# Kernel tuning notes

Measured on AMD Instinct MI355X. Metric: run time of the kernel, lower is better.

Reference implementation:

```python
import jax, jax.numpy as jnp
import numpy as np

L = 2          # layer_num
B = 8192       # nframes * nloc
NNEI = 128
EMB = 128
HID = 128
SHIFT = 20.0   # attnw_shift default
SCALING = (HID * 1.0) ** (-0.5)
LN_EPS = 1e-5


def _l2norm(x):
    # torch F.normalize: x / max(||x||, 1e-12)
    n = jnp.sqrt(jnp.sum(x * x, axis=-1, keepdims=True))
    return x / jnp.maximum(n, 1e-12)


def _layernorm(x, g, b):
    mu = jnp.mean(x, axis=-1, keepdims=True)
    var = jnp.mean((x - mu) ** 2, axis=-1, keepdims=True)
    return (x - mu) * jax.lax.rsqrt(var + LN_EPS) * g + b


def setup_inputs() -> dict:
    key = jax.random.key(0)
    ks = jax.random.split(key, 10)
    input_G = jax.random.normal(ks[0], (B, NNEI, EMB), dtype=jnp.float32)
    nei_mask = jax.random.randint(ks[1], (B, NNEI), 0, 2) > 0
    input_r = jax.random.normal(ks[2], (B, NNEI, 3), dtype=jnp.float32)
    input_r = _l2norm(input_r)  # normalized radial vectors
    sw = jax.random.uniform(ks[3], (B, NNEI), dtype=jnp.float32)
    s = 0.02
    W_in = jax.random.normal(ks[4], (L, EMB, 3 * HID), dtype=jnp.float32) * s
    b_in = jnp.zeros((L, 3 * HID), dtype=jnp.float32)
    W_out = jax.random.normal(ks[5], (L, HID, EMB), dtype=jnp.float32) * s
    b_out = jnp.zeros((L, EMB), dtype=jnp.float32)
    ln_g = jnp.ones((L, EMB), dtype=jnp.float32)
    ln_b = jnp.zeros((L, EMB), dtype=jnp.float32)
    return {"input_G": input_G, "nei_mask": nei_mask, "input_r": input_r,
            "sw": sw, "W_in": W_in, "b_in": b_in, "W_out": W_out,
            "b_out": b_out, "ln_g": ln_g, "ln_b": ln_b}


def reference(input_G, nei_mask, input_r, sw, W_in, b_in, W_out, b_out, ln_g, ln_b):
    # smooth=True, dotr=True path of NeighborGatedAttention
    sw_ij = sw[:, :, None] * sw[:, None, :]                     # [B, nnei, nnei]
    ang = jnp.einsum('bnc,bmc->bnm', input_r, input_r)          # angular weight
    x = input_G
    for l in range(L):
        residual = x
        qkv = jnp.einsum('bne,eh->bnh', x, W_in[l]) + b_in[l]
        q, k, v = jnp.split(qkv, 3, axis=-1)
        q = _l2norm(q) * SCALING
        k = _l2norm(k)
        v = _l2norm(v)
        attn = jnp.einsum('bnh,bmh->bnm', q, k)
        attn = (attn + SHIFT) * sw_ij - SHIFT                   # switch smoothing
        attn = jax.nn.softmax(attn, axis=-1)
        attn = jnp.where(nei_mask[:, :, None], attn, 0.0)       # zero masked rows
        attn = attn * sw_ij * ang                               # smooth + dotr
        o = jnp.einsum('bnm,bmh->bnh', attn, v)
        out = jnp.einsum('bnh,he->bne', o, W_out[l]) + b_out[l]
        x = _layernorm(residual + out, ln_g[l], ln_b[l])
    return x
```

## Files before the change

### kernel.cpp

```cpp
#include <hip/hip_runtime.h>
#include <hip/hip_bf16.h>
#include <math.h>


typedef __attribute__((ext_vector_type(8))) short bf16x8;
typedef __attribute__((ext_vector_type(4))) float f32x4;
typedef unsigned short ushort_t;

constexpr float F_SHIFT   = 20.0f;
constexpr float F_SCALING = 0.08838834764831845f;
constexpr float F_LNEPS   = 1e-5f;

constexpr int ROWP = 136;
constexpr int BUF_US = 128 * ROWP;
constexpr size_t WTI_ELEMS = 2 * 384 * 128;
constexpr size_t WTO_ELEMS = 2 * 128 * 128;
constexpr int TAB_F = 1920;
constexpr int LDS_BYTES = 4 * BUF_US * 2 + 2 * TAB_F * 4;

#define MFMA(a, b, c) __builtin_amdgcn_mfma_f32_16x16x32_bf16(a, b, c, 0, 0, 0)

__device__ __forceinline__ ushort_t f2bf(float f) {
  __hip_bfloat16 h = __float2bfloat16(f);
  return *reinterpret_cast<ushort_t*>(&h);
}
__device__ __forceinline__ ushort4 pack4(float a, float b, float c, float d) {
  return make_ushort4(f2bf(a), f2bf(b), f2bf(c), f2bf(d));
}

template <bool WS>
__device__ __forceinline__ bf16x8 wt_frag(const ushort_t* __restrict__ wt,
                                          const float* __restrict__ W,
                                          int r, int c, int ldW) {
  if constexpr (WS) {
    return *(const bf16x8*)(wt + r * 128 + c);
  } else {
    bf16x8 f;
#pragma unroll
    for (int j = 0; j < 8; ++j) f[j] = (short)f2bf(W[(size_t)(c + j) * ldW + r]);
    return f;
  }
}

__global__ void prep_weights(const float* __restrict__ Win, const float* __restrict__ Wout,
                             ushort_t* __restrict__ wtI, ushort_t* __restrict__ wtO) {
  const int i = blockIdx.x * 256 + threadIdx.x;
  if (i < (int)WTI_ELEMS) {
    const int l = i / (384 * 128), r = i % (384 * 128), h = r >> 7, e = r & 127;
    wtI[i] = f2bf(Win[l * (128 * 384) + e * 384 + h]);
  }
  if (i < (int)WTO_ELEMS) {
    const int l = i >> 14, r = i & 16383, e = r >> 7, h = r & 127;
    wtO[i] = f2bf(Wout[(l << 14) + h * 128 + e]);
  }
}

__device__ __forceinline__ bf16x8 load_xf(const float* xr) {
  const float4 a = *(const float4*)xr;
  const float4 c = *(const float4*)(xr + 4);
  bf16x8 f;
  f[0] = (short)f2bf(a.x); f[1] = (short)f2bf(a.y);
  f[2] = (short)f2bf(a.z); f[3] = (short)f2bf(a.w);
  f[4] = (short)f2bf(c.x); f[5] = (short)f2bf(c.y);
  f[6] = (short)f2bf(c.z); f[7] = (short)f2bf(c.w);
  return f;
}

template <bool WS>
__global__ __launch_bounds__(512, 2)
void ngatt_dual(const float* __restrict__ G, const int* __restrict__ nmask,
                const float* __restrict__ r3, const float* __restrict__ swg,
                const float* __restrict__ Win, const float* __restrict__ bin,
                const float* __restrict__ Wout, const float* __restrict__ bout,
                const float* __restrict__ lng, const float* __restrict__ lnb,
                const ushort_t* __restrict__ wtin, const ushort_t* __restrict__ wtout,
                float* __restrict__ xout) {
  extern __shared__ char smem[];
  ushort_t* bufA0 = (ushort_t*)smem;
  ushort_t* bufB0 = bufA0 + BUF_US;
  ushort_t* bufA1 = bufB0 + BUF_US;
  ushort_t* bufB1 = bufA1 + BUF_US;
  float* tab0 = (float*)(bufB1 + BUF_US);
  float* tab1 = tab0 + TAB_F;

  const int bid = blockIdx.x, t = threadIdx.x;
  const int w = t >> 6, l = t & 63, lc = l & 15, lg = l >> 4;
  const int b0 = 2 * bid, b1 = b0 + 1;
  const size_t bb0 = (size_t)b0 * (128 * 128);
  const size_t bb1 = (size_t)b1 * (128 * 128);
  const int n_mine = 16 * w + lc;

  if (t < 256) {
    const int tb = t >> 7, tt = t & 127;
    float* T = tb ? tab1 : tab0;
    const size_t gi = (size_t)(b0 + tb) * 128 + tt;
    T[1280 + tt] = swg[gi];
    T[1408 + tt] = nmask[gi] ? 1.0f : 0.0f;
    T[1536 + tt] = r3[gi * 3 + 0];
    T[1664 + tt] = r3[gi * 3 + 1];
    T[1792 + tt] = r3[gi * 3 + 2];
  }
  __syncthreads();

  for (int layer = 0; layer < 2; ++layer) {
    const float* xsrc0 = layer ? (xout + bb0) : (G + bb0);
    const float* xsrc1 = layer ? (xout + bb1) : (G + bb1);
    const ushort_t* wtI = wtin + (size_t)layer * 384 * 128;
    const ushort_t* wtO = wtout + (size_t)layer * 128 * 128;
    const float* WinL  = Win  + (size_t)layer * 128 * 384;
    const float* WoutL = Wout + (size_t)layer * 128 * 128;
    const float* binL  = bin  + layer * 384;
    const float* boutL = bout + layer * 128;
    const float* lngL  = lng  + layer * 128;
    const float* lnbL  = lnb  + layer * 128;

    bf16x8 xf0[4], xf1[4];
#pragma unroll
    for (int kk = 0; kk < 4; ++kk) {
      xf0[kk] = load_xf(xsrc0 + (size_t)n_mine * 128 + 8 * lg + 32 * kk);
      xf1[kk] = load_xf(xsrc1 + (size_t)n_mine * 128 + 8 * lg + 32 * kk);
    }

    float ssq0 = 0.f, ssq1 = 0.f, ssk0 = 0.f, ssk1 = 0.f;
#pragma unroll 2
    for (int i = 0; i < 8; ++i) {
      bf16x8 aw[4];
#pragma unroll
      for (int kk = 0; kk < 4; ++kk)
        aw[kk] = wt_frag<WS>(wtI, WinL, 16 * i + lc, 8 * lg + 32 * kk, 384);
      f32x4 a0 = {0, 0, 0, 0}, a1 = {0, 0, 0, 0};
#pragma unroll
      for (int kk = 0; kk < 4; ++kk) {
        a0 = MFMA(aw[kk], xf0[kk], a0);
        a1 = MFMA(aw[kk], xf1[kk], a1);
      }
      const float4 bi = *(const float4*)&binL[16 * i + 4 * lg];
      {
        const float v0 = a0[0] + bi.x, v1 = a0[1] + bi.y, v2 = a0[2] + bi.z, v3 = a0[3] + bi.w;
        ssq0 += v0 * v0 + v1 * v1 + v2 * v2 + v3 * v3;
        *(ushort4*)(bufA0 + n_mine * ROWP + 16 * i + 4 * lg) = pack4(v0, v1, v2, v3);
      }
      {
        const float v0 = a1[0] + bi.x, v1 = a1[1] + bi.y, v2 = a1[2] + bi.z, v3 = a1[3] + bi.w;
        ssq1 += v0 * v0 + v1 * v1 + v2 * v2 + v3 * v3;
        *(ushort4*)(bufA1 + n_mine * ROWP + 16 * i + 4 * lg) = pack4(v0, v1, v2, v3);
      }
    }
#pragma unroll 2
    for (int i = 0; i < 8; ++i) {
      bf16x8 aw[4];
#pragma unroll
      for (int kk = 0; kk < 4; ++kk)
        aw[kk] = wt_frag<WS>(wtI, WinL, 128 + 16 * i + lc, 8 * lg + 32 * kk, 384);
      f32x4 a0 = {0, 0, 0, 0}, a1 = {0, 0, 0, 0};
#pragma unroll
      for (int kk = 0; kk < 4; ++kk) {
        a0 = MFMA(aw[kk], xf0[kk], a0);
        a1 = MFMA(aw[kk], xf1[kk], a1);
      }
      const float4 bi = *(const float4*)&binL[128 + 16 * i + 4 * lg];
      {
        const float v0 = a0[0] + bi.x, v1 = a0[1] + bi.y, v2 = a0[2] + bi.z, v3 = a0[3] + bi.w;
        ssk0 += v0 * v0 + v1 * v1 + v2 * v2 + v3 * v3;
        *(ushort4*)(bufB0 + n_mine * ROWP + 16 * i + 4 * lg) = pack4(v0, v1, v2, v3);
      }
      {
        const float v0 = a1[0] + bi.x, v1 = a1[1] + bi.y, v2 = a1[2] + bi.z, v3 = a1[3] + bi.w;
        ssk1 += v0 * v0 + v1 * v1 + v2 * v2 + v3 * v3;
        *(ushort4*)(bufB1 + n_mine * ROWP + 16 * i + 4 * lg) = pack4(v0, v1, v2, v3);
      }
    }
    ssq0 += __shfl_xor(ssq0, 16); ssq0 += __shfl_xor(ssq0, 32);
    ssq1 += __shfl_xor(ssq1, 16); ssq1 += __shfl_xor(ssq1, 32);
    ssk0 += __shfl_xor(ssk0, 16); ssk0 += __shfl_xor(ssk0, 32);
    ssk1 += __shfl_xor(ssk1, 16); ssk1 += __shfl_xor(ssk1, 32);
    if (l < 16) {
      tab0[0 + n_mine] = ssq0; tab0[128 + n_mine] = ssk0;
      tab1[0 + n_mine] = ssq1; tab1[128 + n_mine] = ssk1;
    }
    __syncthreads();

    if (t < 256) {
      const int tb = t >> 7, tt = t & 127;
      float* T = tb ? tab1 : tab0;
      T[0 + tt] = 1.0f / fmaxf(sqrtf(T[0 + tt]), 1e-12f);
      T[512 + 4 * tt + 0] = (1.0f / fmaxf(sqrtf(T[128 + tt]), 1e-12f)) * F_SCALING;
      T[512 + 4 * tt + 1] = T[1280 + tt];
      T[512 + 4 * tt + 2] = 0.0f;
      T[512 + 4 * tt + 3] = T[1536 + tt];
      T[1024 + 2 * tt + 0] = T[1664 + tt];
      T[1024 + 2 * tt + 1] = T[1792 + tt];
    }
    bf16x8 qf0[4], qf1[4];
#pragma unroll
    for (int kk = 0; kk < 4; ++kk) {
      qf0[kk] = *(const bf16x8*)(bufA0 + n_mine * ROWP + 8 * lg + 32 * kk);
      qf1[kk] = *(const bf16x8*)(bufA1 + n_mine * ROWP + 8 * lg + 32 * kk);
    }
    __syncthreads();

    float ssv0 = 0.f, ssv1 = 0.f;
#pragma unroll 2
    for (int i = 0; i < 8; ++i) {
      bf16x8 aw[4];
#pragma unroll
      for (int kk = 0; kk < 4; ++kk)
        aw[kk] = wt_frag<WS>(wtI, WinL, 256 + 16 * i + lc, 8 * lg + 32 * kk, 384);
      f32x4 a0 = {0, 0, 0, 0}, a1 = {0, 0, 0, 0};
#pragma unroll
      for (int kk = 0; kk < 4; ++kk) {
        a0 = MFMA(aw[kk], xf0[kk], a0);
        a1 = MFMA(aw[kk], xf1[kk], a1);
      }
      const float4 bi = *(const float4*)&binL[256 + 16 * i + 4 * lg];
      {
        const float v0 = a0[0] + bi.x, v1 = a0[1] + bi.y, v2 = a0[2] + bi.z, v3 = a0[3] + bi.w;
        ssv0 += v0 * v0 + v1 * v1 + v2 * v2 + v3 * v3;
        *(ushort4*)(bufA0 + n_mine * ROWP + 16 * i + 4 * lg) = pack4(v0, v1, v2, v3);
      }
      {
        const float v0 = a1[0] + bi.x, v1 = a1[1] + bi.y, v2 = a1[2] + bi.z, v3 = a1[3] + bi.w;
        ssv1 += v0 * v0 + v1 * v1 + v2 * v2 + v3 * v3;
        *(ushort4*)(bufA1 + n_mine * ROWP + 16 * i + 4 * lg) = pack4(v0, v1, v2, v3);
      }
    }
    ssv0 += __shfl_xor(ssv0, 16); ssv0 += __shfl_xor(ssv0, 32);
    ssv1 += __shfl_xor(ssv1, 16); ssv1 += __shfl_xor(ssv1, 32);
    if (l < 16) { tab0[256 + n_mine] = ssv0; tab1[256 + n_mine] = ssv1; }

    ushort4 p0[8], p1[8];
    {
      const float iqn = tab0[0 + n_mine];
      const float swn = tab0[1280 + n_mine];
      const float rxn = tab0[1536 + n_mine], ryn = tab0[1664 + n_mine], rzn = tab0[1792 + n_mine];
      float sum = 0.0f;
      f32x4 sacc[8];
#pragma unroll 2
      for (int mt = 0; mt < 8; ++mt) {
        bf16x8 kf[4];
#pragma unroll
        for (int kk = 0; kk < 4; ++kk)
          kf[kk] = *(const bf16x8*)(bufB0 + (16 * mt + lc) * ROWP + 8 * lg + 32 * kk);
        __builtin_amdgcn_s_setprio(1);
        f32x4 a = {0, 0, 0, 0};
#pragma unroll
        for (int kk = 0; kk < 4; ++kk) a = MFMA(kf[kk], qf0[kk], a);
        __builtin_amdgcn_s_setprio(0);
#pragma unroll
        for (int r2 = 0; r2 < 4; ++r2) {
          const int m = 16 * mt + 4 * lg + r2;
          const float4 a4 = *(const float4*)&tab0[512 + 4 * m];
          const float2 b2 = *(const float2*)&tab0[1024 + 2 * m];
          const float sws = swn * a4.y;
          const float e = __expf((a[r2] * iqn * a4.x + F_SHIFT) * sws - F_SHIFT);
          sum += e;
          a[r2] = e * sws * (rxn * a4.w + ryn * b2.x + rzn * b2.y);
        }
        sacc[mt] = a;
      }
      sum += __shfl_xor(sum, 16); sum += __shfl_xor(sum, 32);
      const float fac = tab0[1408 + n_mine] / sum;
#pragma unroll
      for (int mt = 0; mt < 8; ++mt)
        p0[mt] = pack4(sacc[mt][0] * fac, sacc[mt][1] * fac, sacc[mt][2] * fac, sacc[mt][3] * fac);
    }
    {
      const float iqn = tab1[0 + n_mine];
      const float swn = tab1[1280 + n_mine];
      const float rxn = tab1[1536 + n_mine], ryn = tab1[1664 + n_mine], rzn = tab1[1792 + n_mine];
      float sum = 0.0f;
      f32x4 sacc[8];
#pragma unroll 2
      for (int mt = 0; mt < 8; ++mt) {
        bf16x8 kf[4];
#pragma unroll
        for (int kk = 0; kk < 4; ++kk)
          kf[kk] = *(const bf16x8*)(bufB1 + (16 * mt + lc) * ROWP + 8 * lg + 32 * kk);
        __builtin_amdgcn_s_setprio(1);
        f32x4 a = {0, 0, 0, 0};
#pragma unroll
        for (int kk = 0; kk < 4; ++kk) a = MFMA(kf[kk], qf1[kk], a);
        __builtin_amdgcn_s_setprio(0);
#pragma unroll
        for (int r2 = 0; r2 < 4; ++r2) {
          const int m = 16 * mt + 4 * lg + r2;
          const float4 a4 = *(const float4*)&tab1[512 + 4 * m];
          const float2 b2 = *(const float2*)&tab1[1024 + 2 * m];
          const float sws = swn * a4.y;
          const float e = __expf((a[r2] * iqn * a4.x + F_SHIFT) * sws - F_SHIFT);
          sum += e;
          a[r2] = e * sws * (rxn * a4.w + ryn * b2.x + rzn * b2.y);
        }
        sacc[mt] = a;
      }
      sum += __shfl_xor(sum, 16); sum += __shfl_xor(sum, 32);
      const float fac = tab1[1408 + n_mine] / sum;
#pragma unroll
      for (int mt = 0; mt < 8; ++mt)
        p1[mt] = pack4(sacc[mt][0] * fac, sacc[mt][1] * fac, sacc[mt][2] * fac, sacc[mt][3] * fac);
    }
    __syncthreads();

    if (t < 256) {
      const int tb = t >> 7, tt = t & 127;
      float* T = tb ? tab1 : tab0;
      T[384 + tt] = 1.0f / fmaxf(sqrtf(T[256 + tt]), 1e-12f);
    }
#pragma unroll
    for (int mt = 0; mt < 8; ++mt) {
      *(ushort4*)(bufB0 + n_mine * ROWP + 16 * mt + 4 * lg) = p0[mt];
      *(ushort4*)(bufB1 + n_mine * ROWP + 16 * mt + 4 * lg) = p1[mt];
    }
    bf16x8 vf0[4], vf1[4];
#pragma unroll
    for (int kk = 0; kk < 4; ++kk) {
      vf0[kk] = *(const bf16x8*)(bufA0 + n_mine * ROWP + 8 * lg + 32 * kk);
      vf1[kk] = *(const bf16x8*)(bufA1 + n_mine * ROWP + 8 * lg + 32 * kk);
    }
    __syncthreads();

    {
      const float4 iv0 = *(const float4*)&tab0[384 + 16 * w + 4 * lg];
      const float4 iv1 = *(const float4*)&tab1[384 + 16 * w + 4 * lg];
#pragma unroll 2
      for (int i = 0; i < 8; ++i) {
        bf16x8 bw[4];
#pragma unroll
        for (int kk = 0; kk < 4; ++kk)
          bw[kk] = wt_frag<WS>(wtO, WoutL, 16 * i + lc, 8 * lg + 32 * kk, 128);
        f32x4 a0 = {0, 0, 0, 0}, a1 = {0, 0, 0, 0};
#pragma unroll
        for (int kk = 0; kk < 4; ++kk) {
          a0 = MFMA(vf0[kk], bw[kk], a0);
          a1 = MFMA(vf1[kk], bw[kk], a1);
        }
        *(ushort4*)(bufA0 + (16 * i + lc) * ROWP + 16 * w + 4 * lg) =
            pack4(a0[0] * iv0.x, a0[1] * iv0.y, a0[2] * iv0.z, a0[3] * iv0.w);
        *(ushort4*)(bufA1 + (16 * i + lc) * ROWP + 16 * w + 4 * lg) =
            pack4(a1[0] * iv1.x, a1[1] * iv1.y, a1[2] * iv1.z, a1[3] * iv1.w);
      }
    }
    __syncthreads();

    float bo8[8], g8[8], be8[8];
#pragma unroll
    for (int ct = 0; ct < 8; ++ct) {
      const int e = 16 * ct + lc;
      bo8[ct] = boutL[e]; g8[ct] = lngL[e]; be8[ct] = lnbL[e];
    }
#pragma unroll 1
    for (int which = 0; which < 2; ++which) {
      const ushort_t* bufA = which ? bufA1 : bufA0;
      const ushort_t* bufB = which ? bufB1 : bufB0;
      const float* xsrc = which ? xsrc1 : xsrc0;
      float* xo = xout + (which ? bb1 : bb0);

      float xr8[4][8];
#pragma unroll
      for (int r2 = 0; r2 < 4; ++r2) {
        const float* xr = xsrc + (size_t)(16 * w + 4 * lg + r2) * 128;
#pragma unroll
        for (int ct = 0; ct < 8; ++ct) xr8[r2][ct] = xr[16 * ct + lc];
      }

      bf16x8 pf[4];
#pragma unroll
      for (int kk = 0; kk < 4; ++kk)
        pf[kk] = *(const bf16x8*)(bufB + n_mine * ROWP + 8 * lg + 32 * kk);

      f32x4 oacc[8];
#pragma unroll 2
      for (int i = 0; i < 8; ++i) {
        bf16x8 bf[4];
#pragma unroll
        for (int kk = 0; kk < 4; ++kk)
          bf[kk] = *(const bf16x8*)(bufA + (16 * i + lc) * ROWP + 8 * lg + 32 * kk);
        __builtin_amdgcn_s_setprio(1);
        f32x4 a = {0, 0, 0, 0};
#pragma unroll
        for (int kk = 0; kk < 4; ++kk) a = MFMA(pf[kk], bf[kk], a);
        __builtin_amdgcn_s_setprio(0);
        oacc[i] = a;
      }
#pragma unroll
      for (int r2 = 0; r2 < 4; ++r2) {
        const int n = 16 * w + 4 * lg + r2;
        float vals[8];
        float s1 = 0.0f, s2 = 0.0f;
#pragma unroll
        for (int ct = 0; ct < 8; ++ct) {
          const float v = oacc[ct][r2] + bo8[ct] + xr8[r2][ct];
          vals[ct] = v; s1 += v; s2 += v * v;
        }
        s1 += __shfl_xor(s1, 1); s1 += __shfl_xor(s1, 2);
        s1 += __shfl_xor(s1, 4); s1 += __shfl_xor(s1, 8);
        s2 += __shfl_xor(s2, 1); s2 += __shfl_xor(s2, 2);
        s2 += __shfl_xor(s2, 4); s2 += __shfl_xor(s2, 8);
        const float mu = s1 * (1.0f / 128.0f);
        const float rs = rsqrtf(s2 * (1.0f / 128.0f) - mu * mu + F_LNEPS);
        float* orow = xo + (size_t)n * 128;
#pragma unroll
        for (int ct = 0; ct < 8; ++ct)
          orow[16 * ct + lc] = (vals[ct] - mu) * rs * g8[ct] + be8[ct];
      }
    }
    __syncthreads();
  }
}

extern "C" void kernel_launch(void* const* d_in, const int* in_sizes, int n_in,
                              void* d_out, int out_size, void* d_ws, size_t ws_size,
                              hipStream_t stream) {
  const float* G    = (const float*)d_in[0];
  const int*   msk  = (const int*)d_in[1];
  const float* r3   = (const float*)d_in[2];
  const float* swg  = (const float*)d_in[3];
  const float* Win  = (const float*)d_in[4];
  const float* bin  = (const float*)d_in[5];
  const float* Wout = (const float*)d_in[6];
  const float* bout = (const float*)d_in[7];
  const float* lng  = (const float*)d_in[8];
  const float* lnb  = (const float*)d_in[9];
  float* xout = (float*)d_out;

  const int B = in_sizes[0] / (128 * 128);
  const int nblk = B / 2;
  const bool ws_ok = ws_size >= (WTI_ELEMS + WTO_ELEMS) * sizeof(ushort_t);
  ushort_t* wtI = (ushort_t*)d_ws;
  ushort_t* wtO = wtI + WTI_ELEMS;

  if (ws_ok) {
    prep_weights<<<dim3(384), dim3(256), 0, stream>>>(Win, Wout, wtI, wtO);
    hipFuncSetAttribute(reinterpret_cast<const void*>(ngatt_dual<true>),
                        hipFuncAttributeMaxDynamicSharedMemorySize, LDS_BYTES);
    ngatt_dual<true><<<dim3(nblk), dim3(512), LDS_BYTES, stream>>>(
        G, msk, r3, swg, Win, bin, Wout, bout, lng, lnb, wtI, wtO, xout);
  } else {
    hipFuncSetAttribute(reinterpret_cast<const void*>(ngatt_dual<false>),
                        hipFuncAttributeMaxDynamicSharedMemorySize, LDS_BYTES);
    ngatt_dual<false><<<dim3(nblk), dim3(512), LDS_BYTES, stream>>>(
        G, msk, r3, swg, Win, bin, Wout, bout, lng, lnb, nullptr, nullptr, xout);
  }
}
```

Baseline: 1.680 ms.

## Fold V projection into W_out and drop the separate output projection GEMM

Precomputes W_v·W_out (and b_v·W_out) in the prep kernel, so V' = x·(W_v W_out) is built directly and the attention-times-V' product yields the output projection. The per-row V norm is still computed from the plain V projection and folded into the attention probabilities as a per-key scale. This removes one 128x128 GEMM stage and one block barrier per layer, and also drops the non-workspace fallback path. In exchange the V norms need an extra projection pass, and rounding the fused weights to bf16 slightly changes the numerics.

Result: slower. 1.730 ms (+3.0%).

```diff
diff --git a/kernel.cpp b/kernel.cpp
--- a/kernel.cpp
+++ b/kernel.cpp
@@ -14,7 +14,7 @@
 constexpr int ROWP = 136;
 constexpr int BUF_US = 128 * ROWP;
 constexpr size_t WTI_ELEMS = 2 * 384 * 128;
-constexpr size_t WTO_ELEMS = 2 * 128 * 128;
+constexpr size_t WTW_ELEMS = 2 * 128 * 128;
 constexpr int TAB_F = 1920;
 constexpr int LDS_BYTES = 4 * BUF_US * 2 + 2 * TAB_F * 4;
 
@@ -28,30 +28,32 @@
   return make_ushort4(f2bf(a), f2bf(b), f2bf(c), f2bf(d));
 }
 
-template <bool WS>
-__device__ __forceinline__ bf16x8 wt_frag(const ushort_t* __restrict__ wt,
-                                          const float* __restrict__ W,
-                                          int r, int c, int ldW) {
-  if constexpr (WS) {
-    return *(const bf16x8*)(wt + r * 128 + c);
-  } else {
-    bf16x8 f;
-#pragma unroll
-    for (int j = 0; j < 8; ++j) f[j] = (short)f2bf(W[(size_t)(c + j) * ldW + r]);
-    return f;
-  }
-}
-
 __global__ void prep_weights(const float* __restrict__ Win, const float* __restrict__ Wout,
-                             ushort_t* __restrict__ wtI, ushort_t* __restrict__ wtO) {
+                             const float* __restrict__ bin,
+                             ushort_t* __restrict__ wtI, ushort_t* __restrict__ wtW,
+                             float* __restrict__ bvW) {
   const int i = blockIdx.x * 256 + threadIdx.x;
   if (i < (int)WTI_ELEMS) {
     const int l = i / (384 * 128), r = i % (384 * 128), h = r >> 7, e = r & 127;
     wtI[i] = f2bf(Win[l * (128 * 384) + e * 384 + h]);
   }
-  if (i < (int)WTO_ELEMS) {
-    const int l = i >> 14, r = i & 16383, e = r >> 7, h = r & 127;
-    wtO[i] = f2bf(Wout[(l << 14) + h * 128 + e]);
+  if (i < (int)WTW_ELEMS) {
+    const int l = i >> 14, r = i & 16383, e = r >> 7, k = r & 127;
+    const float* wv = Win + (size_t)l * (128 * 384) + (size_t)k * 384 + 256;
+    const float* wo = Wout + (size_t)l * (128 * 128) + e;
+    float s = 0.f;
+#pragma unroll 8
+    for (int h = 0; h < 128; ++h) s += wv[h] * wo[(size_t)h * 128];
+    wtW[i] = f2bf(s);
+  }
+  if (i < 256) {
+    const int l = i >> 7, e = i & 127;
+    const float* bv = bin + l * 384 + 256;
+    const float* wo = Wout + (size_t)l * (128 * 128) + e;
+    float s = 0.f;
+#pragma unroll 8
+    for (int h = 0; h < 128; ++h) s += bv[h] * wo[(size_t)h * 128];
+    bvW[i] = s;
   }
 }
 
@@ -66,15 +68,13 @@
   return f;
 }
 
-template <bool WS>
 __global__ __launch_bounds__(512, 2)
-void ngatt_dual(const float* __restrict__ G, const int* __restrict__ nmask,
-                const float* __restrict__ r3, const float* __restrict__ swg,
-                const float* __restrict__ Win, const float* __restrict__ bin,
-                const float* __restrict__ Wout, const float* __restrict__ bout,
-                const float* __restrict__ lng, const float* __restrict__ lnb,
-                const ushort_t* __restrict__ wtin, const ushort_t* __restrict__ wtout,
-                float* __restrict__ xout) {
+void ngatt_fused(const float* __restrict__ G, const int* __restrict__ nmask,
+                 const float* __restrict__ r3, const float* __restrict__ swg,
+                 const float* __restrict__ bin, const float* __restrict__ bout,
+                 const float* __restrict__ lng, const float* __restrict__ lnb,
+                 const ushort_t* __restrict__ wtin, const ushort_t* __restrict__ wtw,
+                 const float* __restrict__ bvw, float* __restrict__ xout) {
   extern __shared__ char smem[];
   ushort_t* bufA0 = (ushort_t*)smem;
   ushort_t* bufB0 = bufA0 + BUF_US;
@@ -94,11 +94,15 @@
     const int tb = t >> 7, tt = t & 127;
     float* T = tb ? tab1 : tab0;
     const size_t gi = (size_t)(b0 + tb) * 128 + tt;
-    T[1280 + tt] = swg[gi];
+    const float sw = swg[gi];
+    const float rx = r3[gi * 3 + 0], ry = r3[gi * 3 + 1], rz = r3[gi * 3 + 2];
+    T[1280 + tt] = sw;
     T[1408 + tt] = nmask[gi] ? 1.0f : 0.0f;
-    T[1536 + tt] = r3[gi * 3 + 0];
-    T[1664 + tt] = r3[gi * 3 + 1];
-    T[1792 + tt] = r3[gi * 3 + 2];
+    T[1536 + tt] = rx; T[1664 + tt] = ry; T[1792 + tt] = rz;
+    T[512 + 4 * tt + 1] = sw;
+    T[512 + 4 * tt + 3] = rx;
+    T[1024 + 2 * tt + 0] = ry;
+    T[1024 + 2 * tt + 1] = rz;
   }
   __syncthreads();
 
@@ -106,13 +110,12 @@
     const float* xsrc0 = layer ? (xout + bb0) : (G + bb0);
     const float* xsrc1 = layer ? (xout + bb1) : (G + bb1);
     const ushort_t* wtI = wtin + (size_t)layer * 384 * 128;
-    const ushort_t* wtO = wtout + (size_t)layer * 128 * 128;
-    const float* WinL  = Win  + (size_t)layer * 128 * 384;
-    const float* WoutL = Wout + (size_t)layer * 128 * 128;
-    const float* binL  = bin  + layer * 384;
+    const ushort_t* wtW = wtw + (size_t)layer * 128 * 128;
+    const float* bWl  = bvw + layer * 128;
+    const float* binL = bin + layer * 384;
     const float* boutL = bout + layer * 128;
-    const float* lngL  = lng  + layer * 128;
-    const float* lnbL  = lnb  + layer * 128;
+    const float* lngL = lng + layer * 128;
+    const float* lnbL = lnb + layer * 128;
 
     bf16x8 xf0[4], xf1[4];
 #pragma unroll
@@ -121,13 +124,13 @@
       xf1[kk] = load_xf(xsrc1 + (size_t)n_mine * 128 + 8 * lg + 32 * kk);
     }
 
-    float ssq0 = 0.f, ssq1 = 0.f, ssk0 = 0.f, ssk1 = 0.f;
+    float ssq0 = 0.f, ssq1 = 0.f, ssk0 = 0.f, ssk1 = 0.f, ssv0 = 0.f, ssv1 = 0.f;
 #pragma unroll 2
     for (int i = 0; i < 8; ++i) {
       bf16x8 aw[4];
 #pragma unroll
       for (int kk = 0; kk < 4; ++kk)
-        aw[kk] = wt_frag<WS>(wtI, WinL, 16 * i + lc, 8 * lg + 32 * kk, 384);
+        aw[kk] = *(const bf16x8*)(wtI + (16 * i + lc) * 128 + 8 * lg + 32 * kk);
       f32x4 a0 = {0, 0, 0, 0}, a1 = {0, 0, 0, 0};
 #pragma unroll
       for (int kk = 0; kk < 4; ++kk) {
@@ -151,7 +154,7 @@
       bf16x8 aw[4];
 #pragma unroll
       for (int kk = 0; kk < 4; ++kk)
-        aw[kk] = wt_frag<WS>(wtI, WinL, 128 + 16 * i + lc, 8 * lg + 32 * kk, 384);
+        aw[kk] = *(const bf16x8*)(wtI + (128 + 16 * i + lc) * 128 + 8 * lg + 32 * kk);
       f32x4 a0 = {0, 0, 0, 0}, a1 = {0, 0, 0, 0};
 #pragma unroll
       for (int kk = 0; kk < 4; ++kk) {
@@ -168,28 +171,43 @@
         const float v0 = a1[0] + bi.x, v1 = a1[1] + bi.y, v2 = a1[2] + bi.z, v3 = a1[3] + bi.w;
         ssk1 += v0 * v0 + v1 * v1 + v2 * v2 + v3 * v3;
         *(ushort4*)(bufB1 + n_mine * ROWP + 16 * i + 4 * lg) = pack4(v0, v1, v2, v3);
+      }
+    }
+#pragma unroll 2
+    for (int i = 0; i < 8; ++i) {
+      bf16x8 aw[4];
+#pragma unroll
+      for (int kk = 0; kk < 4; ++kk)
+        aw[kk] = *(const bf16x8*)(wtI + (256 + 16 * i + lc) * 128 + 8 * lg + 32 * kk);
+      f32x4 a0 = {0, 0, 0, 0}, a1 = {0, 0, 0, 0};
+#pragma unroll
+      for (int kk = 0; kk < 4; ++kk) {
+        a0 = MFMA(aw[kk], xf0[kk], a0);
+        a1 = MFMA(aw[kk], xf1[kk], a1);
+      }
+      const float4 bi = *(const float4*)&binL[256 + 16 * i + 4 * lg];
+      {
+        const float v0 = a0[0] + bi.x, v1 = a0[1] + bi.y, v2 = a0[2] + bi.z, v3 = a0[3] + bi.w;
+        ssv0 += v0 * v0 + v1 * v1 + v2 * v2 + v3 * v3;
+      }
+      {
+        const float v0 = a1[0] + bi.x, v1 = a1[1] + bi.y, v2 = a1[2] + bi.z, v3 = a1[3] + bi.w;
+        ssv1 += v0 * v0 + v1 * v1 + v2 * v2 + v3 * v3;
       }
     }
     ssq0 += __shfl_xor(ssq0, 16); ssq0 += __shfl_xor(ssq0, 32);
     ssq1 += __shfl_xor(ssq1, 16); ssq1 += __shfl_xor(ssq1, 32);
     ssk0 += __shfl_xor(ssk0, 16); ssk0 += __shfl_xor(ssk0, 32);
     ssk1 += __shfl_xor(ssk1, 16); ssk1 += __shfl_xor(ssk1, 32);
+    ssv0 += __shfl_xor(ssv0, 16); ssv0 += __shfl_xor(ssv0, 32);
+    ssv1 += __shfl_xor(ssv1, 16); ssv1 += __shfl_xor(ssv1, 32);
     if (l < 16) {
-      tab0[0 + n_mine] = ssq0; tab0[128 + n_mine] = ssk0;
-      tab1[0 + n_mine] = ssq1; tab1[128 + n_mine] = ssk1;
-    }
-    __syncthreads();
-
-    if (t < 256) {
-      const int tb = t >> 7, tt = t & 127;
-      float* T = tb ? tab1 : tab0;
-      T[0 + tt] = 1.0f / fmaxf(sqrtf(T[0 + tt]), 1e-12f);
-      T[512 + 4 * tt + 0] = (1.0f / fmaxf(sqrtf(T[128 + tt]), 1e-12f)) * F_SCALING;
-      T[512 + 4 * tt + 1] = T[1280 + tt];
-      T[512 + 4 * tt + 2] = 0.0f;
-      T[512 + 4 * tt + 3] = T[1536 + tt];
-      T[1024 + 2 * tt + 0] = T[1664 + tt];
-      T[1024 + 2 * tt + 1] = T[1792 + tt];
+      tab0[n_mine] = 1.0f / fmaxf(sqrtf(ssq0), 1e-12f);
+      tab0[512 + 4 * n_mine + 0] = (1.0f / fmaxf(sqrtf(ssk0), 1e-12f)) * F_SCALING;
+      tab0[512 + 4 * n_mine + 2] = 1.0f / fmaxf(sqrtf(ssv0), 1e-12f);
+      tab1[n_mine] = 1.0f / fmaxf(sqrtf(ssq1), 1e-12f);
+      tab1[512 + 4 * n_mine + 0] = (1.0f / fmaxf(sqrtf(ssk1), 1e-12f)) * F_SCALING;
+      tab1[512 + 4 * n_mine + 2] = 1.0f / fmaxf(sqrtf(ssv1), 1e-12f);
     }
     bf16x8 qf0[4], qf1[4];
 #pragma unroll
@@ -199,38 +217,28 @@
     }
     __syncthreads();
 
-    float ssv0 = 0.f, ssv1 = 0.f;
 #pragma unroll 2
     for (int i = 0; i < 8; ++i) {
-      bf16x8 aw[4];
+      bf16x8 ww[4];
 #pragma unroll
       for (int kk = 0; kk < 4; ++kk)
-        aw[kk] = wt_frag<WS>(wtI, WinL, 256 + 16 * i + lc, 8 * lg + 32 * kk, 384);
+        ww[kk] = *(const bf16x8*)(wtW + (16 * i + lc) * 128 + 8 * lg + 32 * kk);
       f32x4 a0 = {0, 0, 0, 0}, a1 = {0, 0, 0, 0};
 #pragma unroll
       for (int kk = 0; kk < 4; ++kk) {
-        a0 = MFMA(aw[kk], xf0[kk], a0);
-        a1 = MFMA(aw[kk], xf1[kk], a1);
-      }
-      const float4 bi = *(const float4*)&binL[256 + 16 * i + 4 * lg];
-      {
-        const float v0 = a0[0] + bi.x, v1 = a0[1] + bi.y, v2 = a0[2] + bi.z, v3 = a0[3] + bi.w;
-        ssv0 += v0 * v0 + v1 * v1 + v2 * v2 + v3 * v3;
-        *(ushort4*)(bufA0 + n_mine * ROWP + 16 * i + 4 * lg) = pack4(v0, v1, v2, v3);
-      }
-      {
-        const float v0 = a1[0] + bi.x, v1 = a1[1] + bi.y, v2 = a1[2] + bi.z, v3 = a1[3] + bi.w;
-        ssv1 += v0 * v0 + v1 * v1 + v2 * v2 + v3 * v3;
-        *(ushort4*)(bufA1 + n_mine * ROWP + 16 * i + 4 * lg) = pack4(v0, v1, v2, v3);
-      }
-    }
-    ssv0 += __shfl_xor(ssv0, 16); ssv0 += __shfl_xor(ssv0, 32);
-    ssv1 += __shfl_xor(ssv1, 16); ssv1 += __shfl_xor(ssv1, 32);
-    if (l < 16) { tab0[256 + n_mine] = ssv0; tab1[256 + n_mine] = ssv1; }
+        a0 = MFMA(xf0[kk], ww[kk], a0);
+        a1 = MFMA(xf1[kk], ww[kk], a1);
+      }
+      const float bv = bWl[16 * i + lc];
+      *(ushort4*)(bufA0 + (16 * i + lc) * ROWP + 16 * w + 4 * lg) =
+          pack4(a0[0] + bv, a0[1] + bv, a0[2] + bv, a0[3] + bv);
+      *(ushort4*)(bufA1 + (16 * i + lc) * ROWP + 16 * w + 4 * lg) =
+          pack4(a1[0] + bv, a1[1] + bv, a1[2] + bv, a1[3] + bv);
+    }
 
     ushort4 p0[8], p1[8];
     {
-      const float iqn = tab0[0 + n_mine];
+      const float iqn = tab0[n_mine];
       const float swn = tab0[1280 + n_mine];
       const float rxn = tab0[1536 + n_mine], ryn = tab0[1664 + n_mine], rzn = tab0[1792 + n_mine];
       float sum = 0.0f;
@@ -254,7 +262,7 @@
           const float sws = swn * a4.y;
           const float e = __expf((a[r2] * iqn * a4.x + F_SHIFT) * sws - F_SHIFT);
           sum += e;
-          a[r2] = e * sws * (rxn * a4.w + ryn * b2.x + rzn * b2.y);
+          a[r2] = e * sws * a4.z * (rxn * a4.w + ryn * b2.x + rzn * b2.y);
         }
         sacc[mt] = a;
       }
@@ -265,7 +273,7 @@
         p0[mt] = pack4(sacc[mt][0] * fac, sacc[mt][1] * fac, sacc[mt][2] * fac, sacc[mt][3] * fac);
     }
     {
-      const float iqn = tab1[0 + n_mine];
+      const float iqn = tab1[n_mine];
       const float swn = tab1[1280 + n_mine];
       const float rxn = tab1[1536 + n_mine], ryn = tab1[1664 + n_mine], rzn = tab1[1792 + n_mine];
       float sum = 0.0f;
@@ -289,7 +297,7 @@
           const float sws = swn * a4.y;
           const float e = __expf((a[r2] * iqn * a4.x + F_SHIFT) * sws - F_SHIFT);
           sum += e;
-          a[r2] = e * sws * (rxn * a4.w + ryn * b2.x + rzn * b2.y);
+          a[r2] = e * sws * a4.z * (rxn * a4.w + ryn * b2.x + rzn * b2.y);
         }
         sacc[mt] = a;
       }
@@ -301,46 +309,11 @@
     }
     __syncthreads();
 
-    if (t < 256) {
-      const int tb = t >> 7, tt = t & 127;
-      float* T = tb ? tab1 : tab0;
-      T[384 + tt] = 1.0f / fmaxf(sqrtf(T[256 + tt]), 1e-12f);
-    }
 #pragma unroll
     for (int mt = 0; mt < 8; ++mt) {
       *(ushort4*)(bufB0 + n_mine * ROWP + 16 * mt + 4 * lg) = p0[mt];
       *(ushort4*)(bufB1 + n_mine * ROWP + 16 * mt + 4 * lg) = p1[mt];
     }
-    bf16x8 vf0[4], vf1[4];
-#pragma unroll
-    for (int kk = 0; kk < 4; ++kk) {
-      vf0[kk] = *(const bf16x8*)(bufA0 + n_mine * ROWP + 8 * lg + 32 * kk);
-      vf1[kk] = *(const bf16x8*)(bufA1 + n_mine * ROWP + 8 * lg + 32 * kk);
-    }
-    __syncthreads();
-
-    {
-      const float4 iv0 = *(const float4*)&tab0[384 + 16 * w + 4 * lg];
-      const float4 iv1 = *(const float4*)&tab1[384 + 16 * w + 4 * lg];
-#pragma unroll 2
-      for (int i = 0; i < 8; ++i) {
-        bf16x8 bw[4];
-#pragma unroll
-        for (int kk = 0; kk < 4; ++kk)
-          bw[kk] = wt_frag<WS>(wtO, WoutL, 16 * i + lc, 8 * lg + 32 * kk, 128);
-        f32x4 a0 = {0, 0, 0, 0}, a1 = {0, 0, 0, 0};
-#pragma unroll
-        for (int kk = 0; kk < 4; ++kk) {
-          a0 = MFMA(vf0[kk], bw[kk], a0);
-          a1 = MFMA(vf1[kk], bw[kk], a1);
-        }
-        *(ushort4*)(bufA0 + (16 * i + lc) * ROWP + 16 * w + 4 * lg) =
-            pack4(a0[0] * iv0.x, a0[1] * iv0.y, a0[2] * iv0.z, a0[3] * iv0.w);
-        *(ushort4*)(bufA1 + (16 * i + lc) * ROWP + 16 * w + 4 * lg) =
-            pack4(a1[0] * iv1.x, a1[1] * iv1.y, a1[2] * iv1.z, a1[3] * iv1.w);
-      }
-    }
-    __syncthreads();
 
     float bo8[8], g8[8], be8[8];
 #pragma unroll
@@ -362,7 +335,6 @@
 #pragma unroll
         for (int ct = 0; ct < 8; ++ct) xr8[r2][ct] = xr[16 * ct + lc];
       }
-
       bf16x8 pf[4];
 #pragma unroll
       for (int kk = 0; kk < 4; ++kk)
@@ -425,20 +397,13 @@
 
   const int B = in_sizes[0] / (128 * 128);
   const int nblk = B / 2;
-  const bool ws_ok = ws_size >= (WTI_ELEMS + WTO_ELEMS) * sizeof(ushort_t);
   ushort_t* wtI = (ushort_t*)d_ws;
-  ushort_t* wtO = wtI + WTI_ELEMS;
-
-  if (ws_ok) {
-    prep_weights<<<dim3(384), dim3(256), 0, stream>>>(Win, Wout, wtI, wtO);
-    hipFuncSetAttribute(reinterpret_cast<const void*>(ngatt_dual<true>),
-                        hipFuncAttributeMaxDynamicSharedMemorySize, LDS_BYTES);
-    ngatt_dual<true><<<dim3(nblk), dim3(512), LDS_BYTES, stream>>>(
-        G, msk, r3, swg, Win, bin, Wout, bout, lng, lnb, wtI, wtO, xout);
-  } else {
-    hipFuncSetAttribute(reinterpret_cast<const void*>(ngatt_dual<false>),
-                        hipFuncAttributeMaxDynamicSharedMemorySize, LDS_BYTES);
-    ngatt_dual<false><<<dim3(nblk), dim3(512), LDS_BYTES, stream>>>(
-        G, msk, r3, swg, Win, bin, Wout, bout, lng, lnb, nullptr, nullptr, xout);
-  }
-}
+  ushort_t* wtW = wtI + WTI_ELEMS;
+  float* bvW = (float*)(wtW + WTW_ELEMS);
+
+  prep_weights<<<dim3(384), dim3(256), 0, stream>>>(Win, Wout, bin, wtI, wtW, bvW);
+  hipFuncSetAttribute(reinterpret_cast<const void*>(ngatt_fused),
+                      hipFuncAttributeMaxDynamicSharedMemorySize, LDS_BYTES);
+  ngatt_fused<<<dim3(nblk), dim3(512), LDS_BYTES, stream>>>(
+      G, msk, r3, swg, bin, bout, lng, lnb, wtI, wtW, bvW, xout);
+}
```
